# Kernel optimization log

Measured on AMD Instinct MI355X. Metric: run time of the kernel, lower is better.

## Reference

```python
import jax, jax.numpy as jnp
import numpy as np

GROUPS = 32
EPS = 1e-5


def _group_norm(x, scale, bias):
    B, C, H, W = x.shape
    xg = x.reshape(B, GROUPS, -1)
    mu = xg.mean(axis=-1, keepdims=True)
    var = jnp.mean(jnp.square(xg - mu), axis=-1, keepdims=True)
    xn = ((xg - mu) * jax.lax.rsqrt(var + EPS)).reshape(B, C, H, W)
    return xn * scale[None, :, None, None] + bias[None, :, None, None]


def _conv1x1(x, w, b):
    # x: [B,C,H,W], w: [O,C], b: [O]
    return jnp.einsum('bchw,oc->bohw', x, w) + b[None, :, None, None]


def setup_inputs() -> dict:
    key = jax.random.key(0)
    ks = jax.random.split(key, 6)
    B, C, H, W = 16, 512, 32, 32
    x = jax.random.normal(ks[0], (B, C, H, W), dtype=jnp.float32)
    # xavier_uniform for [C, C, 1, 1] conv: limit = sqrt(6 / (fan_in + fan_out)) = sqrt(6 / (2C))
    lim = float(np.sqrt(6.0 / (2 * C)))
    wq = jax.random.uniform(ks[1], (C, C), jnp.float32, -lim, lim)
    wk = jax.random.uniform(ks[2], (C, C), jnp.float32, -lim, lim)
    wv = jax.random.uniform(ks[3], (C, C), jnp.float32, -lim, lim)
    wo = jax.random.uniform(ks[4], (C, C), jnp.float32, -lim, lim) * 1e-5  # gain=1e-5
    zeros_c = jnp.zeros((C,), jnp.float32)
    return {
        'x': x,
        'gn_scale': jnp.ones((C,), jnp.float32),
        'gn_bias': zeros_c,
        'wq': wq, 'bq': zeros_c,
        'wk': wk, 'bk': zeros_c,
        'wv': wv, 'bv': zeros_c,
        'wo': wo, 'bo': zeros_c,
    }


def reference(x, gn_scale, gn_bias, wq, bq, wk, bk, wv, bv, wo, bo):
    B, C, H, W = x.shape
    N = H * W
    h = _group_norm(x, gn_scale, gn_bias)
    q = _conv1x1(h, wq, bq).reshape(B, C, N)  # [B,C,N]
    k = _conv1x1(h, wk, bk).reshape(B, C, N)
    v = _conv1x1(h, wv, bv).reshape(B, C, N)
    scale = 1.0 / jnp.sqrt(jnp.asarray(C, x.dtype))
    w = jnp.einsum('bcn,bcm->bnm', q, k) * scale  # [B,N,N]
    w = jax.nn.softmax(w, axis=-1)
    hv = jnp.einsum('bnm,bcm->bcn', w, v).reshape(B, C, H, W)
    out = _conv1x1(hv, wo, bo)
    return x + out
```

## Files before the change

kernel.cpp:

```cpp
#include <hip/hip_runtime.h>
#include <hip/hip_bf16.h>
#include <cstdint>

typedef __bf16 bf16;
typedef unsigned char u8;
typedef __bf16 bf16x8 __attribute__((ext_vector_type(8)));
typedef __bf16 bf16x4 __attribute__((ext_vector_type(4)));
typedef float floatx4 __attribute__((ext_vector_type(4)));
typedef float floatx2 __attribute__((ext_vector_type(2)));
typedef int intx8 __attribute__((ext_vector_type(8)));

__device__ __forceinline__ void gld_lds16(const void* g, void* l) {
    __builtin_amdgcn_global_load_lds(
        (const __attribute__((address_space(1))) unsigned int*)g,
        (__attribute__((address_space(3))) unsigned int*)l, 16, 0, 0);
}

__device__ __forceinline__ u8 f2fp8(float v) {
    return (u8)(__builtin_amdgcn_cvt_pk_fp8_f32(v, v, 0, false) & 0xff);
}
__device__ __forceinline__ unsigned int pack4_fp8(float a, float b, float c, float d) {
    unsigned int u = __builtin_amdgcn_cvt_pk_fp8_f32(a, b, 0, false);
    u = __builtin_amdgcn_cvt_pk_fp8_f32(c, d, u, true);
    return u;
}

__device__ __forceinline__ intx8 ld_frag(const u8* p, int lo, int hi) {
    uint4 a = *(const uint4*)(p + lo);
    uint4 b = *(const uint4*)(p + hi);
    intx8 r;
    r[0] = a.x; r[1] = a.y; r[2] = a.z; r[3] = a.w;
    r[4] = b.x; r[5] = b.y; r[6] = b.z; r[7] = b.w;
    return r;
}

__global__ __launch_bounds__(256) void setup_kernel(
    const float* __restrict__ x, const float* __restrict__ gs,
    const float* __restrict__ gb,
    const float* __restrict__ wq, const float* __restrict__ wk,
    const float* __restrict__ wv, const float* __restrict__ wo,
    const float* __restrict__ bq, const float* __restrict__ bk,
    const float* __restrict__ bv,
    u8* __restrict__ hT, u8* __restrict__ wqkv, u8* __restrict__ wob,
    float* __restrict__ bqkv)
{
    const int t = threadIdx.x;
    if (blockIdx.x >= 512) {
        int i = (blockIdx.x - 512) * 256 + t;
        if (i < 786432) {
            int which = i >> 18;
            int off = i & 262143;
            const float* src = which == 0 ? wq : which == 1 ? wk : wv;
            wqkv[i] = f2fp8(src[off]);
        } else {
            wob[i - 786432] = f2fp8(wo[i - 786432] * 262144.0f);
        }
        if (i < 1536)
            bqkv[i] = i < 512 ? bq[i] : (i < 1024 ? bk[i - 512] : bv[i - 1024]);
        return;
    }
    const int b = blockIdx.x >> 5;
    const int g = blockIdx.x & 31;
    const int wave = t >> 6, lane = t & 63;
    const float4* x4 = (const float4*)(x + ((long long)b * 512 + g * 16) * 1024);

    float4 v[16];
    float s1 = 0.f, s2 = 0.f;
#pragma unroll
    for (int i = 0; i < 16; ++i) {
        v[i] = x4[i * 256 + t];
        s1 += v[i].x + v[i].y + v[i].z + v[i].w;
        s2 += v[i].x * v[i].x + v[i].y * v[i].y + v[i].z * v[i].z + v[i].w * v[i].w;
    }
#pragma unroll
    for (int m = 32; m; m >>= 1) {
        s1 += __shfl_xor(s1, m, 64);
        s2 += __shfl_xor(s2, m, 64);
    }
    __shared__ float red[2][4];
    __shared__ float stats[2];
    if (lane == 0) { red[0][wave] = s1; red[1][wave] = s2; }
    __syncthreads();
    if (t == 0) {
        float a = red[0][0] + red[0][1] + red[0][2] + red[0][3];
        float q = red[1][0] + red[1][1] + red[1][2] + red[1][3];
        float mu = a * (1.0f / 16384.0f);
        float var = q * (1.0f / 16384.0f) - mu * mu;
        stats[0] = mu;
        stats[1] = rsqrtf(var + 1e-5f);
    }
    __syncthreads();
    const float mu = stats[0], rs = stats[1];

#pragma unroll
    for (int i = 0; i < 16; ++i) {
        const float sc = gs[g * 16 + i] * rs;
        const float bi = gb[g * 16 + i] - mu * sc;
        v[i].x = v[i].x * sc + bi;
        v[i].y = v[i].y * sc + bi;
        v[i].z = v[i].z * sc + bi;
        v[i].w = v[i].w * sc + bi;
    }
    u8* hb = hT + (long long)b * 524288 + g * 16;
#pragma unroll
    for (int r = 0; r < 4; ++r) {
        uint4 o;
        o.x = pack4_fp8(v[0][r],  v[1][r],  v[2][r],  v[3][r]);
        o.y = pack4_fp8(v[4][r],  v[5][r],  v[6][r],  v[7][r]);
        o.z = pack4_fp8(v[8][r],  v[9][r],  v[10][r], v[11][r]);
        o.w = pack4_fp8(v[12][r], v[13][r], v[14][r], v[15][r]);
        *(uint4*)(hb + (long long)(4 * t + r) * 512) = o;
    }
}

template <int EPI>
__global__ __launch_bounds__(256, 3) void gemm_mx(
    const u8* __restrict__ A, long long sA,
    const u8* __restrict__ B, long long sB,
    void* __restrict__ C, long long sC,
    void* __restrict__ C2, void* __restrict__ C3,
    int ldC, int K,
    const float* __restrict__ bias,
    const float* __restrict__ resid, long long sR,
    float scale)
{
    __shared__ __align__(16) u8 smem[33792];
    const int tid = threadIdx.x;
    const int l = tid & 63;
    const int wave = tid >> 6;
    const int wm = wave >> 1, wn = wave & 1;
    const int bm = blockIdx.x, bn = blockIdx.y, b = blockIdx.z;

    const u8* Ab = A + (long long)b * sA + (long long)bm * 128 * K;
    const u8* Bb = B + (long long)b * sB + (long long)bn * 128 * K;

    const int srow = wave * 8 + (l >> 3);
    const int sg = ((l & 7) ^ ((l >> 3) & 7)) * 16;
    const u8* ga  = Ab + (long long)srow * K + sg;
    const u8* gbp = Bb + (long long)srow * K + sg;
    const long long c32 = (long long)32 * K;
    const int ldst = wave * 1024;

    const int q4 = l >> 4;
    const int glo = ((2 * q4) ^ (l & 7)) * 16;
    const int ghi = ((2 * q4 + 1) ^ (l & 7)) * 16;
    int arow[4], brow[4];
#pragma unroll
    for (int i = 0; i < 4; ++i) {
        arow[i] = (wm * 64 + i * 16 + (l & 15)) * 128;
        brow[i] = (wn * 64 + i * 16 + (l & 15)) * 128 + 16384;
    }

    floatx4 acc[4][4] = {};
    const int niter = K >> 7;

    for (int it = 0; it < niter; ++it) {
        const int k0 = it << 7;
#pragma unroll
        for (int c = 0; c < 4; ++c) {
            gld_lds16(ga + c * c32 + k0, smem + c * 4096 + ldst);
            gld_lds16(gbp + c * c32 + k0, smem + 16384 + c * 4096 + ldst);
        }
        __syncthreads();
        intx8 bfr[4];
#pragma unroll
        for (int j = 0; j < 4; ++j) bfr[j] = ld_frag(smem + brow[j], glo, ghi);
#pragma unroll
        for (int i = 0; i < 4; ++i) {
            intx8 af = ld_frag(smem + arow[i], glo, ghi);
#pragma unroll
            for (int j = 0; j < 4; ++j)
                acc[i][j] = __builtin_amdgcn_mfma_scale_f32_16x16x128_f8f6f4(
                    af, bfr[j], acc[i][j], 0, 0, 0, 127, 0, 127);
        }
        __syncthreads();
    }

    if (EPI == 3) {
        float* Cf = (float*)C;
#pragma unroll
        for (int i = 0; i < 4; ++i) {
            const int mrow = bm * 128 + wm * 64 + i * 16 + (l >> 4) * 4;
#pragma unroll
            for (int j = 0; j < 4; ++j) {
                const int ncol = bn * 128 + wn * 64 + j * 16 + (l & 15);
#pragma unroll
                for (int r = 0; r < 4; ++r) {
                    const int row = mrow + r;
                    float v = acc[i][j][r] * scale + bias[row] +
                              resid[(long long)b * sR + (long long)row * ldC + ncol];
                    Cf[(long long)b * sC + (long long)row * ldC + ncol] = v;
                }
            }
        }
    } else if (EPI == 1) {
        const int which = bn >> 2;
        u8* tile = smem;
#pragma unroll
        for (int i = 0; i < 4; ++i) {
            const int rl = wm * 64 + i * 16 + (l >> 4) * 4;
#pragma unroll
            for (int j = 0; j < 4; ++j) {
                const int cl = wn * 64 + j * 16 + (l & 15);
                const float badd = bias[bn * 128 + cl];
                if (which == 2) {
                    *(unsigned int*)(tile + cl * 144 + rl) =
                        pack4_fp8(acc[i][j][0] + badd, acc[i][j][1] + badd,
                                  acc[i][j][2] + badd, acc[i][j][3] + badd);
                } else {
#pragma unroll
                    for (int r = 0; r < 4; ++r)
                        tile[(rl + r) * 144 + cl] = f2fp8(acc[i][j][r] + badd);
                }
            }
        }
        __syncthreads();
        const int slot = (tid & 7) * 16;
#pragma unroll
        for (int p = 0; p < 4; ++p) {
            const int row = p * 32 + (tid >> 3);
            uint4 d = *(const uint4*)(tile + row * 144 + slot);
            u8* dst;
            if (which == 0)
                dst = (u8*)C + (long long)b * sC + (long long)(bm * 128 + row) * 512
                      + (bn & 3) * 128 + slot;
            else if (which == 1)
                dst = (u8*)C2 + (long long)b * sC + (long long)(bm * 128 + row) * 512
                      + (bn & 3) * 128 + slot;
            else
                dst = (u8*)C3 + (long long)b * sC + (long long)((bn & 3) * 128 + row) * 1024
                      + bm * 128 + slot;
            *(uint4*)dst = d;
        }
    } else {
        u8* tile = smem;
#pragma unroll
        for (int i = 0; i < 4; ++i) {
            const int rl = wm * 64 + i * 16 + (l >> 4) * 4;
#pragma unroll
            for (int j = 0; j < 4; ++j) {
                const int cl = wn * 64 + j * 16 + (l & 15);
#pragma unroll
                for (int r = 0; r < 4; ++r)
                    tile[(rl + r) * 144 + cl] = f2fp8(acc[i][j][r] * scale);
            }
        }
        __syncthreads();
        const int slot = (tid & 7) * 16;
#pragma unroll
        for (int p = 0; p < 4; ++p) {
            const int row = p * 32 + (tid >> 3);
            uint4 d = *(const uint4*)(tile + row * 144 + slot);
            u8* dst = (u8*)C + (long long)b * sC + (long long)(bm * 128 + row) * ldC
                      + bn * 128 + slot;
            *(uint4*)dst = d;
        }
    }
}

__global__ __launch_bounds__(256) void softmax_kernel(
    const u8* __restrict__ S, u8* __restrict__ P)
{
    const int wave = threadIdx.x >> 6, lane = threadIdx.x & 63;
    const long long row = (long long)blockIdx.x * 4 + wave;
    uint4 d = *(const uint4*)(S + row * 1024 + lane * 16);
    float v[16];
#pragma unroll
    for (int h = 0; h < 4; ++h) {
        const unsigned w = h == 0 ? d.x : h == 1 ? d.y : h == 2 ? d.z : d.w;
        floatx2 lo = __builtin_amdgcn_cvt_pk_f32_fp8(w, false);
        floatx2 hi = __builtin_amdgcn_cvt_pk_f32_fp8(w, true);
        v[h * 4 + 0] = lo[0]; v[h * 4 + 1] = lo[1];
        v[h * 4 + 2] = hi[0]; v[h * 4 + 3] = hi[1];
    }
    float m = v[0];
#pragma unroll
    for (int i = 1; i < 16; ++i) m = fmaxf(m, v[i]);
#pragma unroll
    for (int k = 32; k; k >>= 1) m = fmaxf(m, __shfl_xor(m, k, 64));
    float s = 0.f;
#pragma unroll
    for (int i = 0; i < 16; ++i) { v[i] = __expf(0.25f * (v[i] - m)); s += v[i]; }
#pragma unroll
    for (int k = 32; k; k >>= 1) s += __shfl_xor(s, k, 64);
    const float r = 64.0f / s;
    uint4 o;
    o.x = pack4_fp8(v[0] * r, v[1] * r, v[2] * r, v[3] * r);
    o.y = pack4_fp8(v[4] * r, v[5] * r, v[6] * r, v[7] * r);
    o.z = pack4_fp8(v[8] * r, v[9] * r, v[10] * r, v[11] * r);
    o.w = pack4_fp8(v[12] * r, v[13] * r, v[14] * r, v[15] * r);
    *(uint4*)(P + row * 1024 + lane * 16) = o;
}

extern "C" void kernel_launch(void* const* d_in, const int* in_sizes, int n_in,
                              void* d_out, int out_size, void* d_ws, size_t ws_size,
                              hipStream_t stream)
{
    const float* x  = (const float*)d_in[0];
    const float* gs = (const float*)d_in[1];
    const float* gb = (const float*)d_in[2];
    const float* wq = (const float*)d_in[3];
    const float* bq = (const float*)d_in[4];
    const float* wk = (const float*)d_in[5];
    const float* bk = (const float*)d_in[6];
    const float* wv = (const float*)d_in[7];
    const float* bv = (const float*)d_in[8];
    const float* wo = (const float*)d_in[9];
    const float* bo = (const float*)d_in[10];
    float* out = (float*)d_out;

    u8* p = (u8*)d_ws;
    u8* hT   = p; p += 8388608;
    u8* q    = p; p += 8388608;
    u8* k    = p; p += 8388608;
    u8* v    = p; p += 8388608;
    u8* wqkv = p; p += 786432;
    float* bqkv = (float*)p; p += 6144;
    u8* wob  = p; p += 262144;
    u8* S    = p; p += 16777216;
    u8* P    = p; p += 16777216;
    u8* hvT  = p; p += 8388608;

    setup_kernel<<<4608, 256, 0, stream>>>(x, gs, gb, wq, wk, wv, wo, bq, bk, bv,
                                           hT, wqkv, wob, bqkv);

    gemm_mx<1><<<dim3(8, 12, 16), 256, 0, stream>>>(
        hT, 524288LL, wqkv, 0LL, q, 524288LL, k, v,
        512, 512, bqkv, nullptr, 0LL, 1.0f);
    gemm_mx<2><<<dim3(8, 8, 16), 256, 0, stream>>>(
        q, 524288LL, k, 524288LL, S, 1048576LL, nullptr, nullptr,
        1024, 512, nullptr, nullptr, 0LL, 0.17677669529663687f);
    softmax_kernel<<<4096, 256, 0, stream>>>(S, P);
    gemm_mx<2><<<dim3(8, 4, 16), 256, 0, stream>>>(
        P, 1048576LL, v, 524288LL, hvT, 524288LL, nullptr, nullptr,
        512, 1024, nullptr, nullptr, 0LL, 0.015625f);
    gemm_mx<3><<<dim3(4, 8, 16), 256, 0, stream>>>(
        wob, 0LL, hvT, 524288LL, out, 524288LL, nullptr, nullptr,
        1024, 512, bo, x, 524288LL, 3.814697265625e-06f);
}
```

Measured before the change: 180.2 us.

## Fuse softmax exponentiation into the QK GEMM epilogue and defer normalization

```diff
diff --git a/kernel.cpp b/kernel.cpp
--- a/kernel.cpp
+++ b/kernel.cpp
@@ -2,12 +2,8 @@
 #include <hip/hip_bf16.h>
 #include <cstdint>
 
-typedef __bf16 bf16;
 typedef unsigned char u8;
-typedef __bf16 bf16x8 __attribute__((ext_vector_type(8)));
-typedef __bf16 bf16x4 __attribute__((ext_vector_type(4)));
 typedef float floatx4 __attribute__((ext_vector_type(4)));
-typedef float floatx2 __attribute__((ext_vector_type(2)));
 typedef int intx8 __attribute__((ext_vector_type(8)));
 
 __device__ __forceinline__ void gld_lds16(const void* g, void* l) {
@@ -42,7 +38,7 @@
     const float* __restrict__ bq, const float* __restrict__ bk,
     const float* __restrict__ bv,
     u8* __restrict__ hT, u8* __restrict__ wqkv, u8* __restrict__ wob,
-    float* __restrict__ bqkv)
+    float* __restrict__ bqkv, float* __restrict__ lsum)
 {
     const int t = threadIdx.x;
     if (blockIdx.x >= 512) {
@@ -57,6 +53,8 @@
         }
         if (i < 1536)
             bqkv[i] = i < 512 ? bq[i] : (i < 1024 ? bk[i - 512] : bv[i - 1024]);
+        if (i < 16384)
+            lsum[i] = 0.0f;
         return;
     }
     const int b = blockIdx.x >> 5;
@@ -122,7 +120,7 @@
     int ldC, int K,
     const float* __restrict__ bias,
     const float* __restrict__ resid, long long sR,
-    float scale)
+    float scale, float* __restrict__ lsum)
 {
     __shared__ __align__(16) u8 smem[33792];
     const int tid = threadIdx.x;
@@ -180,7 +178,7 @@
         float* Cf = (float*)C;
 #pragma unroll
         for (int i = 0; i < 4; ++i) {
-            const int mrow = bm * 128 + wm * 64 + i * 16 + (l >> 4) * 4;
+            const int mrow = bm * 128 + wm * 64 + i * 16 + q4 * 4;
 #pragma unroll
             for (int j = 0; j < 4; ++j) {
                 const int ncol = bn * 128 + wn * 64 + j * 16 + (l & 15);
@@ -198,7 +196,7 @@
         u8* tile = smem;
 #pragma unroll
         for (int i = 0; i < 4; ++i) {
-            const int rl = wm * 64 + i * 16 + (l >> 4) * 4;
+            const int rl = wm * 64 + i * 16 + q4 * 4;
 #pragma unroll
             for (int j = 0; j < 4; ++j) {
                 const int cl = wn * 64 + j * 16 + (l & 15);
@@ -232,17 +230,31 @@
                       + bm * 128 + slot;
             *(uint4*)dst = d;
         }
-    } else {
+    } else if (EPI == 4) {
         u8* tile = smem;
 #pragma unroll
         for (int i = 0; i < 4; ++i) {
-            const int rl = wm * 64 + i * 16 + (l >> 4) * 4;
+            const int rl = wm * 64 + i * 16 + q4 * 4;
+            float psum[4] = {0.f, 0.f, 0.f, 0.f};
 #pragma unroll
             for (int j = 0; j < 4; ++j) {
                 const int cl = wn * 64 + j * 16 + (l & 15);
 #pragma unroll
-                for (int r = 0; r < 4; ++r)
-                    tile[(rl + r) * 144 + cl] = f2fp8(acc[i][j][r] * scale);
+                for (int r = 0; r < 4; ++r) {
+                    float e = __expf(acc[i][j][r] * scale);
+                    psum[r] += e;
+                    tile[(rl + r) * 144 + cl] = f2fp8(e * 0.25f);
+                }
+            }
+#pragma unroll
+            for (int r = 0; r < 4; ++r) {
+#pragma unroll
+                for (int m = 8; m; m >>= 1) psum[r] += __shfl_xor(psum[r], m, 64);
+            }
+            if ((l & 15) == 0) {
+                float* lp = lsum + b * 1024 + bm * 128 + rl;
+#pragma unroll
+                for (int r = 0; r < 4; ++r) atomicAdd(lp + r, psum[r]);
             }
         }
         __syncthreads();
@@ -255,41 +267,34 @@
                       + bn * 128 + slot;
             *(uint4*)dst = d;
         }
-    }
-}
-
-__global__ __launch_bounds__(256) void softmax_kernel(
-    const u8* __restrict__ S, u8* __restrict__ P)
-{
-    const int wave = threadIdx.x >> 6, lane = threadIdx.x & 63;
-    const long long row = (long long)blockIdx.x * 4 + wave;
-    uint4 d = *(const uint4*)(S + row * 1024 + lane * 16);
-    float v[16];
-#pragma unroll
-    for (int h = 0; h < 4; ++h) {
-        const unsigned w = h == 0 ? d.x : h == 1 ? d.y : h == 2 ? d.z : d.w;
-        floatx2 lo = __builtin_amdgcn_cvt_pk_f32_fp8(w, false);
-        floatx2 hi = __builtin_amdgcn_cvt_pk_f32_fp8(w, true);
-        v[h * 4 + 0] = lo[0]; v[h * 4 + 1] = lo[1];
-        v[h * 4 + 2] = hi[0]; v[h * 4 + 3] = hi[1];
-    }
-    float m = v[0];
-#pragma unroll
-    for (int i = 1; i < 16; ++i) m = fmaxf(m, v[i]);
-#pragma unroll
-    for (int k = 32; k; k >>= 1) m = fmaxf(m, __shfl_xor(m, k, 64));
-    float s = 0.f;
-#pragma unroll
-    for (int i = 0; i < 16; ++i) { v[i] = __expf(0.25f * (v[i] - m)); s += v[i]; }
-#pragma unroll
-    for (int k = 32; k; k >>= 1) s += __shfl_xor(s, k, 64);
-    const float r = 64.0f / s;
-    uint4 o;
-    o.x = pack4_fp8(v[0] * r, v[1] * r, v[2] * r, v[3] * r);
-    o.y = pack4_fp8(v[4] * r, v[5] * r, v[6] * r, v[7] * r);
-    o.z = pack4_fp8(v[8] * r, v[9] * r, v[10] * r, v[11] * r);
-    o.w = pack4_fp8(v[12] * r, v[13] * r, v[14] * r, v[15] * r);
-    *(uint4*)(P + row * 1024 + lane * 16) = o;
+    } else {
+        u8* tile = smem;
+#pragma unroll
+        for (int i = 0; i < 4; ++i) {
+            const int rl = wm * 64 + i * 16 + q4 * 4;
+            const float* lp = lsum + b * 1024 + bm * 128 + rl;
+            float rc[4];
+#pragma unroll
+            for (int r = 0; r < 4; ++r) rc[r] = 4.0f / lp[r];
+#pragma unroll
+            for (int j = 0; j < 4; ++j) {
+                const int cl = wn * 64 + j * 16 + (l & 15);
+#pragma unroll
+                for (int r = 0; r < 4; ++r)
+                    tile[(rl + r) * 144 + cl] = f2fp8(acc[i][j][r] * rc[r]);
+            }
+        }
+        __syncthreads();
+        const int slot = (tid & 7) * 16;
+#pragma unroll
+        for (int p = 0; p < 4; ++p) {
+            const int row = p * 32 + (tid >> 3);
+            uint4 d = *(const uint4*)(tile + row * 144 + slot);
+            u8* dst = (u8*)C + (long long)b * sC + (long long)(bm * 128 + row) * ldC
+                      + bn * 128 + slot;
+            *(uint4*)dst = d;
+        }
+    }
 }
 
 extern "C" void kernel_launch(void* const* d_in, const int* in_sizes, int n_in,
@@ -317,24 +322,23 @@
     u8* wqkv = p; p += 786432;
     float* bqkv = (float*)p; p += 6144;
     u8* wob  = p; p += 262144;
-    u8* S    = p; p += 16777216;
     u8* P    = p; p += 16777216;
     u8* hvT  = p; p += 8388608;
+    float* lsum = (float*)p; p += 65536;
 
     setup_kernel<<<4608, 256, 0, stream>>>(x, gs, gb, wq, wk, wv, wo, bq, bk, bv,
-                                           hT, wqkv, wob, bqkv);
+                                           hT, wqkv, wob, bqkv, lsum);
 
     gemm_mx<1><<<dim3(8, 12, 16), 256, 0, stream>>>(
         hT, 524288LL, wqkv, 0LL, q, 524288LL, k, v,
-        512, 512, bqkv, nullptr, 0LL, 1.0f);
-    gemm_mx<2><<<dim3(8, 8, 16), 256, 0, stream>>>(
-        q, 524288LL, k, 524288LL, S, 1048576LL, nullptr, nullptr,
-        1024, 512, nullptr, nullptr, 0LL, 0.17677669529663687f);
-    softmax_kernel<<<4096, 256, 0, stream>>>(S, P);
-    gemm_mx<2><<<dim3(8, 4, 16), 256, 0, stream>>>(
+        512, 512, bqkv, nullptr, 0LL, 1.0f, nullptr);
+    gemm_mx<4><<<dim3(8, 8, 16), 256, 0, stream>>>(
+        q, 524288LL, k, 524288LL, P, 1048576LL, nullptr, nullptr,
+        1024, 512, nullptr, nullptr, 0LL, 0.044194173824159216f, lsum);
+    gemm_mx<5><<<dim3(8, 4, 16), 256, 0, stream>>>(
         P, 1048576LL, v, 524288LL, hvT, 524288LL, nullptr, nullptr,
-        512, 1024, nullptr, nullptr, 0LL, 0.015625f);
+        512, 1024, nullptr, nullptr, 0LL, 1.0f, lsum);
     gemm_mx<3><<<dim3(4, 8, 16), 256, 0, stream>>>(
         wob, 0LL, hvT, 524288LL, out, 524288LL, nullptr, nullptr,
-        1024, 512, bo, x, 524288LL, 3.814697265625e-06f);
-}
+        1024, 512, bo, x, 524288LL, 3.814697265625e-06f, nullptr);
+}
```

Result: no change. 176.7 us (-1.9%).
